# Kernel tuning notes

Hardware: AMD Instinct MI355X
Metric: run time of the kernel (lower is better)

The kernel has to match this reference:

```python
import jax, jax.numpy as jnp
import numpy as np

B, N, D, H = 2, 2048, 1024, 16
DH = D // H
MASK_VALUE = -1e7


def setup_inputs() -> dict:
    key = jax.random.key(0)
    ks = jax.random.split(key, 8)
    scale = 0.02
    return {
        "queries": jax.random.normal(ks[0], (B, N, D), dtype=jnp.float32),
        "keys": jax.random.normal(ks[1], (B, N, D), dtype=jnp.float32),
        "values": jax.random.normal(ks[2], (B, N, D), dtype=jnp.float32),
        "valid_len": jax.random.randint(ks[3], (B * H,), 1, N + 1, dtype=jnp.int32),
        "Wq": jax.random.normal(ks[4], (D, D), dtype=jnp.float32) * scale,
        "Wk": jax.random.normal(ks[5], (D, D), dtype=jnp.float32) * scale,
        "Wv": jax.random.normal(ks[6], (D, D), dtype=jnp.float32) * scale,
        "Wo": jax.random.normal(ks[7], (D, D), dtype=jnp.float32) * scale,
    }


def reference(queries, keys, values, valid_len, Wq, Wk, Wv, Wo):
    b, n, d = queries.shape
    h, dh = H, d // H

    def split_heads(x):  # (b, n, d) -> (b, h, n, dh)
        return x.reshape(b, n, h, dh).transpose(0, 2, 1, 3)

    q = split_heads(queries @ Wq)
    k = split_heads(keys @ Wk)
    v = split_heads(values @ Wv)

    # (b, h, nq, nk) full score tensor, as in the original naive bmm path
    scores = jnp.einsum("bhqd,bhkd->bhqk", q, k) / jnp.sqrt(jnp.float32(dh))

    # valid_len is 1-D of length b*h; repeat_interleave over queries means the
    # mask depends only on the key index: keep k < valid_len[bh]
    vl = valid_len.reshape(b, h, 1, 1)
    keep = jnp.arange(n)[None, None, None, :] < vl  # (b, h, 1, nk)
    scores = jnp.where(keep, scores, MASK_VALUE)

    attn = jax.nn.softmax(scores, axis=-1)
    heads = jnp.einsum("bhqk,bhkd->bhqd", attn, v)  # (b, h, n, dh)
    out = heads.transpose(0, 2, 1, 3).reshape(b, n, d) @ Wo
    return out
```

## Files before the change

kernel.cpp:

```cpp
#include <hip/hip_runtime.h>

#define B_ 2
#define N_ 2048
#define D_ 1024
#define H_ 16
#define DH_ 64
#define NITEMS 1024

typedef _Float16 half8 __attribute__((ext_vector_type(8)));
typedef _Float16 half4 __attribute__((ext_vector_type(4)));
typedef _Float16 half2 __attribute__((ext_vector_type(2)));
typedef float f32x4 __attribute__((ext_vector_type(4)));

__device__ __forceinline__ void gl2lds16(const _Float16* g, _Float16* l) {
  __builtin_amdgcn_global_load_lds(
      (const __attribute__((address_space(1))) void*)g,
      (__attribute__((address_space(3))) void*)l, 16, 0, 0);
}

__device__ __forceinline__ half2 cvt_pk_f16(float a, float b) {
  auto r = __builtin_amdgcn_cvt_pkrtz(a, b);
  return __builtin_bit_cast(half2, r);
}

__global__ __launch_bounds__(256) void prep_kernel(
    const float* __restrict__ q, const float* __restrict__ k,
    const float* __restrict__ v, const float* __restrict__ Wq,
    const float* __restrict__ Wk, const float* __restrict__ Wv,
    const float* __restrict__ Wo, const int* __restrict__ vlen,
    _Float16* __restrict__ Xf, _Float16* __restrict__ WtAll,
    int* __restrict__ order) {
  __shared__ float tile[64][65];
  const int bid = blockIdx.x;
  if (bid < 6144) {
    int y = bid >> 11, x = bid & 2047;
    const float* s = (y == 0) ? q : (y == 1) ? k : v;
    _Float16* d = Xf + (size_t)y * ((size_t)B_ * N_ * D_);
    size_t idx = ((size_t)x * 256 + threadIdx.x) * 8;
    float4 a = *(const float4*)(s + idx);
    float4 b = *(const float4*)(s + idx + 4);
    half8 h;
    h[0] = (_Float16)a.x; h[1] = (_Float16)a.y; h[2] = (_Float16)a.z; h[3] = (_Float16)a.w;
    h[4] = (_Float16)b.x; h[5] = (_Float16)b.y; h[6] = (_Float16)b.z; h[7] = (_Float16)b.w;
    *(half8*)(d + idx) = h;
  } else if (bid < 6144 + 1024) {
    int idx = bid - 6144;
    int z = idx >> 8, rem = idx & 255, gy = rem >> 4, gx = rem & 15;
    const float* W = (z == 0) ? Wq : (z == 1) ? Wk : (z == 2) ? Wv : Wo;
    _Float16* Wt = WtAll + (size_t)z * D_ * D_;
    int k0 = gy * 64, n0 = gx * 64;
    int tr = threadIdx.x >> 4, tc = threadIdx.x & 15;
#pragma unroll
    for (int i = 0; i < 4; ++i) {
      int r = tr + i * 16;
      float4 va = *(const float4*)(W + (size_t)(k0 + r) * D_ + n0 + tc * 4);
      tile[r][tc * 4 + 0] = va.x; tile[r][tc * 4 + 1] = va.y;
      tile[r][tc * 4 + 2] = va.z; tile[r][tc * 4 + 3] = va.w;
    }
    __syncthreads();
#pragma unroll
    for (int i = 0; i < 4; ++i) {
      int r = tr + i * 16;
      half4 hv;
      hv[0] = (_Float16)tile[tc * 4 + 0][r];
      hv[1] = (_Float16)tile[tc * 4 + 1][r];
      hv[2] = (_Float16)tile[tc * 4 + 2][r];
      hv[3] = (_Float16)tile[tc * 4 + 3][r];
      *(half4*)(Wt + (size_t)(n0 + r) * D_ + k0 + tc * 4) = hv;
    }
  } else {
    int i = threadIdx.x;
    if (i < B_ * H_) {
      int vi = vlen[i], rank = 0;
      for (int j = 0; j < B_ * H_; ++j) {
        int vj = vlen[j];
        if (vj > vi || (vj == vi && j < i)) ++rank;
      }
      order[rank] = i;
    }
  }
}

#define BK 32

template <int NT, int MODE>
__global__ __launch_bounds__(256) void gemm_f16_kernel(
    const _Float16* __restrict__ Aall, const _Float16* __restrict__ Btall,
    _Float16* __restrict__ ChAll, float* __restrict__ Cf32) {
  constexpr int BN = NT * 32;
  constexpr int K = D_;
  __shared__ __attribute__((aligned(16))) _Float16 As[128 * BK];
  __shared__ __attribute__((aligned(16))) _Float16 Bs[BN * BK];
  const int z = blockIdx.z;
  const _Float16* A  = Aall  + (size_t)z * ((size_t)B_ * N_ * D_);
  const _Float16* Bt = Btall + (size_t)z * ((size_t)D_ * D_);
  _Float16* Chead = ChAll + (size_t)z * ((size_t)B_ * N_ * D_);

  const int tid = threadIdx.x;
  const int m0 = blockIdx.y * 128, n0 = blockIdx.x * BN;
  const int lane = tid & 63, w = tid >> 6;
  const int quad = lane >> 4, l15 = lane & 15;
  const int wm = (w >> 1) * 64, wn = (w & 1) * (BN / 2);
  const int swz = (quad ^ ((l15 >> 1) & 3)) * 8;
  f32x4 acc[4][NT] = {};

  for (int kt = 0; kt < K; kt += BK) {
    if (kt) __syncthreads();
#pragma unroll
    for (int p = 0; p < 2; ++p) {
      int c = p * 256 + tid;
      int row = c >> 2, pg = c & 3;
      int gl = pg ^ ((row >> 1) & 3);
      gl2lds16(A + (size_t)(m0 + row) * K + kt + gl * 8, &As[c * 8]);
    }
#pragma unroll
    for (int p = 0; p < NT / 2; ++p) {
      int c = p * 256 + tid;
      int row = c >> 2, pg = c & 3;
      int gl = pg ^ ((row >> 1) & 3);
      gl2lds16(Bt + (size_t)(n0 + row) * K + kt + gl * 8, &Bs[c * 8]);
    }
    __syncthreads();
    half8 af[4], bf[NT];
#pragma unroll
    for (int mt = 0; mt < 4; ++mt)
      af[mt] = *(const half8*)&As[(wm + mt * 16 + l15) * 32 + swz];
#pragma unroll
    for (int nt = 0; nt < NT; ++nt)
      bf[nt] = *(const half8*)&Bs[(wn + nt * 16 + l15) * 32 + swz];
#pragma unroll
    for (int mt = 0; mt < 4; ++mt)
#pragma unroll
      for (int nt = 0; nt < NT; ++nt)
        acc[mt][nt] = __builtin_amdgcn_mfma_f32_16x16x32_f16(
            af[mt], bf[nt], acc[mt][nt], 0, 0, 0);
  }

#pragma unroll
  for (int mt = 0; mt < 4; ++mt) {
    int mrow = m0 + wm + mt * 16 + quad * 4;
#pragma unroll
    for (int nt = 0; nt < NT; ++nt) {
      int jcol = n0 + wn + nt * 16 + l15;
      if (MODE == 0) {
        int b = mrow >> 11, n = mrow & (N_ - 1);
        int h = jcol >> 6, dh = jcol & (DH_ - 1);
        if (z == 2) {
          half4 o;
#pragma unroll
          for (int r = 0; r < 4; ++r) o[r] = (_Float16)acc[mt][nt][r];
          *(half4*)(ChAll + 2 * (size_t)B_ * N_ * D_ +
                    ((size_t)(b * H_ + h) * DH_ + dh) * N_ + n) = o;
        } else {
          const float scl = (z == 0) ? 0.18033688011112042f : 1.0f;
#pragma unroll
          for (int r = 0; r < 4; ++r)
            Chead[((((size_t)(b * H_ + h)) * N_ + n + r) * DH_) + dh] =
                (_Float16)(acc[mt][nt][r] * scl);
        }
      } else {
#pragma unroll
        for (int r = 0; r < 4; ++r)
          Cf32[(size_t)(mrow + r) * D_ + jcol] = acc[mt][nt][r];
      }
    }
  }
}

__global__ __launch_bounds__(256, 4) void attn_kernel(
    const _Float16* __restrict__ Qh, const _Float16* __restrict__ Kh,
    const _Float16* __restrict__ VtG, const int* __restrict__ vlen,
    _Float16* __restrict__ Hd, const int* __restrict__ order) {
  __shared__ __attribute__((aligned(16))) _Float16 Ks[2][64 * 64];
  __shared__ __attribute__((aligned(16))) _Float16 Vt[2][64 * 64];
  const int tid = threadIdx.x, lane = tid & 63, w = tid >> 6;
  const int quad = lane >> 4, l15 = lane & 15;
  const int sw  = (quad ^ (l15 & 7)) * 8;
  const int sw2 = ((quad + 4) ^ (l15 & 7)) * 8;
  const half4 ones = {(_Float16)1, (_Float16)1, (_Float16)1, (_Float16)1};

  const int item = (blockIdx.x * 331) & (NITEMS - 1);
  const int bh = order[item >> 5];
  const int q0 = (item & 31) * 64;
  const int b = bh >> 4, h = bh & (H_ - 1);
  const int vl = vlen[bh];
  const int KT = (vl + 63) >> 6;
  const _Float16* Qb = Qh  + (size_t)bh * N_ * DH_;
  const _Float16* Kb = Kh  + (size_t)bh * N_ * DH_;
  const _Float16* Vb = VtG + (size_t)bh * N_ * DH_;

  const half8 qb0 = *(const half8*)(Qb + (size_t)(q0 + w * 16 + l15) * DH_ + quad * 8);
  const half8 qb1 = *(const half8*)(Qb + (size_t)(q0 + w * 16 + l15) * DH_ + 32 + quad * 8);

  half8 kpre[2], vpre[2];
  auto prefetch = [&](int k0k) {
#pragma unroll
    for (int p = 0; p < 2; ++p) {
      int c = p * 256 + tid;
      int row = c >> 3, pg = c & 7;
      kpre[p] = *(const half8*)(Kb + (size_t)(k0k + row) * DH_ + (pg ^ (row & 7)) * 8);
      vpre[p] = *(const half8*)(Vb + (size_t)row * N_ + k0k + pg * 8);
    }
  };
  auto commit = [&](int buf) {
#pragma unroll
    for (int p = 0; p < 2; ++p) {
      int c = p * 256 + tid;
      int row = c >> 3, pg = c & 7;
      *(half8*)&Ks[buf][c * 8] = kpre[p];
      int j0 = (pg * 2) ^ (row & 15), j1 = (pg * 2 + 1) ^ (row & 15);
      half4 lo = {vpre[p][0], vpre[p][1], vpre[p][2], vpre[p][3]};
      half4 hi = {vpre[p][4], vpre[p][5], vpre[p][6], vpre[p][7]};
      *(half4*)&Vt[buf][row * 64 + j0 * 4] = lo;
      *(half4*)&Vt[buf][row * 64 + j1 * 4] = hi;
    }
  };

  prefetch(0);
  commit(0);
  if (KT > 1) prefetch(64);
  __syncthreads();

  f32x4 Oacc[4] = {};
  f32x4 lacc = {};

  for (int kt = 0; kt < KT; ++kt) {
    const int cur = kt & 1;
    if (kt + 1 < KT) commit(1 - cur);
    if (kt + 2 < KT) prefetch((kt + 2) * 64);

    f32x4 s[4];
#pragma unroll
    for (int nt = 0; nt < 4; ++nt) {
      int r = nt * 16 + l15;
      half8 ka0 = *(const half8*)&Ks[cur][r * 64 + sw];
      half8 ka1 = *(const half8*)&Ks[cur][r * 64 + sw2];
      f32x4 c = {};
      c = __builtin_amdgcn_mfma_f32_16x16x32_f16(ka0, qb0, c, 0, 0, 0);
      c = __builtin_amdgcn_mfma_f32_16x16x32_f16(ka1, qb1, c, 0, 0, 0);
      s[nt] = c;
    }
    const int k0k = kt * 64;
    half4 pf[4];
    if (k0k + 64 <= vl) {
#pragma unroll
      for (int nt = 0; nt < 4; ++nt) {
        half2 lo = cvt_pk_f16(exp2f(s[nt][0]), exp2f(s[nt][1]));
        half2 hi = cvt_pk_f16(exp2f(s[nt][2]), exp2f(s[nt][3]));
        pf[nt] = __builtin_shufflevector(lo, hi, 0, 1, 2, 3);
      }
    } else {
#pragma unroll
      for (int nt = 0; nt < 4; ++nt) {
        int keyb = k0k + nt * 16 + quad * 4;
#pragma unroll
        for (int r = 0; r < 4; ++r) {
          float p = exp2f(s[nt][r]);
          pf[nt][r] = (keyb + r < vl) ? (_Float16)p : (_Float16)0.f;
        }
      }
    }
#pragma unroll
    for (int nt = 0; nt < 4; ++nt) {
      lacc = __builtin_amdgcn_mfma_f32_16x16x16f16(ones, pf[nt], lacc, 0, 0, 0);
#pragma unroll
      for (int dt = 0; dt < 4; ++dt) {
        int dh = dt * 16 + l15;
        half4 va = *(const half4*)&Vt[cur][dh * 64 + (((nt * 4 + quad) ^ l15) << 2)];
        Oacc[dt] = __builtin_amdgcn_mfma_f32_16x16x16f16(va, pf[nt], Oacc[dt], 0, 0, 0);
      }
    }
    __syncthreads();
  }

  float inv_l = 1.0f / lacc[0];
  int q = q0 + w * 16 + l15;
  _Float16* out = Hd + ((size_t)(b * N_ + q)) * D_ + h * DH_;
#pragma unroll
  for (int dt = 0; dt < 4; ++dt) {
    half4 o;
#pragma unroll
    for (int r = 0; r < 4; ++r) o[r] = (_Float16)(Oacc[dt][r] * inv_l);
    *(half4*)(out + dt * 16 + quad * 4) = o;
  }
}

extern "C" void kernel_launch(void* const* d_in, const int* in_sizes, int n_in,
                              void* d_out, int out_size, void* d_ws, size_t ws_size,
                              hipStream_t stream) {
  const float* q  = (const float*)d_in[0];
  const float* k  = (const float*)d_in[1];
  const float* v  = (const float*)d_in[2];
  const int*   vl = (const int*)d_in[3];
  const float* Wq = (const float*)d_in[4];
  const float* Wk = (const float*)d_in[5];
  const float* Wv = (const float*)d_in[6];
  const float* Wo = (const float*)d_in[7];

  const size_t XSZ = (size_t)B_ * N_ * D_;
  const size_t WSZ = (size_t)D_ * D_;
  _Float16* ws = (_Float16*)d_ws;
  _Float16* Xf = ws;
  _Float16* Wt = Xf + 3 * XSZ;
  _Float16* Qh = Wt + 4 * WSZ;
  _Float16* Hd = Qh + 3 * XSZ;
  int* order = (int*)(Hd + XSZ);

  prep_kernel<<<dim3(6144 + 1024 + 1), 256, 0, stream>>>(
      q, k, v, Wq, Wk, Wv, Wo, vl, Xf, Wt, order);

  gemm_f16_kernel<4, 0><<<dim3(D_ / 128, 32, 3), 256, 0, stream>>>(
      Xf, Wt, Qh, nullptr);

  attn_kernel<<<dim3(NITEMS), 256, 0, stream>>>(
      Qh, Qh + XSZ, Qh + 2 * XSZ, vl, Hd, order);

  gemm_f16_kernel<2, 1><<<dim3(D_ / 64, 32, 1), 256, 0, stream>>>(
      Hd, Wt + 3 * WSZ, nullptr, (float*)d_out);
}
```

Baseline: 224.6 us.

## Map attention blocks to XCDs by head rank; move softmax scale into kernel

Replaces the multiplicative-hash item mapping with an XCD-aware mapping: blockIdx low 3 bits pick the XCD, and each XCD serves a fixed set of four heads chosen by sorted order, so K/V tiles stay resident in that XCD's L2 and load is balanced across XCDs. It also drops the scale applied to Q in the projection epilogue, applying the 1/sqrt(dh)*log2e factor inside the exp2 in the attention loop instead. The packed round-toward-zero conversion is replaced by plain per-element fp16 casts. These add a multiply per score element and change rounding slightly, in exchange for better cache locality and balance.

```diff
diff --git a/kernel.cpp b/kernel.cpp
--- a/kernel.cpp
+++ b/kernel.cpp
@@ -9,18 +9,12 @@
 
 typedef _Float16 half8 __attribute__((ext_vector_type(8)));
 typedef _Float16 half4 __attribute__((ext_vector_type(4)));
-typedef _Float16 half2 __attribute__((ext_vector_type(2)));
 typedef float f32x4 __attribute__((ext_vector_type(4)));
 
 __device__ __forceinline__ void gl2lds16(const _Float16* g, _Float16* l) {
   __builtin_amdgcn_global_load_lds(
       (const __attribute__((address_space(1))) void*)g,
       (__attribute__((address_space(3))) void*)l, 16, 0, 0);
-}
-
-__device__ __forceinline__ half2 cvt_pk_f16(float a, float b) {
-  auto r = __builtin_amdgcn_cvt_pkrtz(a, b);
-  return __builtin_bit_cast(half2, r);
 }
 
 __global__ __launch_bounds__(256) void prep_kernel(
@@ -152,11 +146,10 @@
           *(half4*)(ChAll + 2 * (size_t)B_ * N_ * D_ +
                     ((size_t)(b * H_ + h) * DH_ + dh) * N_ + n) = o;
         } else {
-          const float scl = (z == 0) ? 0.18033688011112042f : 1.0f;
 #pragma unroll
           for (int r = 0; r < 4; ++r)
             Chead[((((size_t)(b * H_ + h)) * N_ + n + r) * DH_) + dh] =
-                (_Float16)(acc[mt][nt][r] * scl);
+                (_Float16)acc[mt][nt][r];
         }
       } else {
 #pragma unroll
@@ -177,11 +170,17 @@
   const int quad = lane >> 4, l15 = lane & 15;
   const int sw  = (quad ^ (l15 & 7)) * 8;
   const int sw2 = ((quad + 4) ^ (l15 & 7)) * 8;
+  const float sc2 = 0.125f * 1.44269504088896f;
   const half4 ones = {(_Float16)1, (_Float16)1, (_Float16)1, (_Float16)1};
 
-  const int item = (blockIdx.x * 331) & (NITEMS - 1);
-  const int bh = order[item >> 5];
-  const int q0 = (item & 31) * 64;
+  const int bid = blockIdx.x;
+  const int xcd = bid & 7;
+  const int wi  = bid >> 3;
+  const int i4 = wi & 3, t = wi >> 2;
+  const int qsel = (i4 + t + (t >> 3)) & 3;
+  const int rank = xcd + 8 * qsel;
+  const int bh = order[rank];
+  const int q0 = t * 64;
   const int b = bh >> 4, h = bh & (H_ - 1);
   const int vl = vlen[bh];
   const int KT = (vl + 63) >> 6;
@@ -244,18 +243,17 @@
     half4 pf[4];
     if (k0k + 64 <= vl) {
 #pragma unroll
-      for (int nt = 0; nt < 4; ++nt) {
-        half2 lo = cvt_pk_f16(exp2f(s[nt][0]), exp2f(s[nt][1]));
-        half2 hi = cvt_pk_f16(exp2f(s[nt][2]), exp2f(s[nt][3]));
-        pf[nt] = __builtin_shufflevector(lo, hi, 0, 1, 2, 3);
-      }
+      for (int nt = 0; nt < 4; ++nt)
+#pragma unroll
+        for (int r = 0; r < 4; ++r)
+          pf[nt][r] = (_Float16)exp2f(s[nt][r] * sc2);
     } else {
 #pragma unroll
       for (int nt = 0; nt < 4; ++nt) {
         int keyb = k0k + nt * 16 + quad * 4;
 #pragma unroll
         for (int r = 0; r < 4; ++r) {
-          float p = exp2f(s[nt][r]);
+          float p = exp2f(s[nt][r] * sc2);
           pf[nt][r] = (keyb + r < vl) ? (_Float16)p : (_Float16)0.f;
         }
       }
```

Measured after the change: 222.2 us. About the same (-1.0%).
